# Optimization experiments

Hardware: AMD Instinct MI355X
Metric: run time of the kernel (lower is better)

The kernel has to match this reference:

```python
import jax, jax.numpy as jnp
import numpy as np

B, C, H, W = 16, 512, 32, 32
HW = H * W  # == input_features == output_features for shapes to be consistent


def setup_inputs() -> dict:
    key = jax.random.key(0)
    k1, k2, k3 = jax.random.split(key, 3)
    node1 = jax.random.normal(k1, (B, C, H, W), dtype=jnp.float32)
    node2 = jax.random.normal(k2, (B, C, H, W), dtype=jnp.float32)
    # nn.Linear(input_features, output_features, bias=False).weight: [out, in]
    W_c = jax.random.normal(k3, (HW, HW), dtype=jnp.float32) * (1.0 / np.sqrt(HW))
    return {"node1": node1, "node2": node2, "W_c": W_c}


def reference(node1, node2, W_c):
    b, c, h, w = node1.shape
    hw = h * w
    n1 = node1.reshape(b, c, hw)  # [B, C, HW]
    n2 = node2.reshape(b, c, hw)  # [B, C, HW]
    # x = W_c(n1): Linear applies y = x @ W^T  -> [B, C, HW_out]
    x = jnp.einsum('bch,oh->bco', n1, W_c)
    # e = bmm(x.permute(0,2,1), n2): [B, HW_out, C] @ [B, C, HW] -> [B, HW_out, HW]
    e = jnp.einsum('bco,bch->boh', x, n2)
    a = jax.nn.softmax(e, axis=-1)  # softmax over last dim (HW of node2)
    # m = bmm(n2, a): [B, C, HW] @ [B, HW, HW] -> [B, C, HW]
    m = jnp.einsum('bck,bkj->bcj', n2, a)
    return m
```

## Files before the change

kernel.cpp:

```cpp
#include <hip/hip_runtime.h>
#include <math.h>


typedef _Float16 f16;
typedef _Float16 f16x8 __attribute__((ext_vector_type(8)));
typedef _Float16 f16x4 __attribute__((ext_vector_type(4)));
typedef float f32x4 __attribute__((ext_vector_type(4)));

#define L2E 1.442695040888963f

#define WG_BARRIER() asm volatile("s_waitcnt lgkmcnt(0)\ns_barrier" ::: "memory")

#define DMA16(g, l)                                                             \
    __builtin_amdgcn_global_load_lds(                                           \
        (const __attribute__((address_space(1))) void*)(g),                     \
        (__attribute__((address_space(3))) void*)(l), 16, 0, 0)

__device__ __forceinline__ f16x8 cvt8(f32x4 lo, f32x4 hi) {
    f16x8 o;
#pragma unroll
    for (int i = 0; i < 4; ++i) { o[i] = (f16)lo[i]; o[4 + i] = (f16)hi[i]; }
    return o;
}

__device__ __forceinline__ f16x8 expb(f16x8 b, f32x4 cl, f32x4 ch) {
    f16x8 t;
#pragma unroll
    for (int i = 0; i < 4; ++i) t[i] = (f16)exp2f(fmaf((float)b[i], L2E, -cl[i]));
#pragma unroll
    for (int i = 0; i < 4; ++i) t[4 + i] = (f16)exp2f(fmaf((float)b[4 + i], L2E, -ch[i]));
    return t;
}

__global__ __launch_bounds__(256) void prep(const float* __restrict__ n1,
                                            const float* __restrict__ Wc,
                                            const float* __restrict__ n2,
                                            f16* __restrict__ n1f, f16* __restrict__ Wf,
                                            f16* __restrict__ n2t) {
    const int bid = blockIdx.x, tid = threadIdx.x;
    if (bid < 4608) {
        const float* s = (bid < 4096) ? n1 : Wc;
        f16* d = (bid < 4096) ? n1f : Wf;
        const size_t i = ((size_t)(bid < 4096 ? bid : bid - 4096) * 256 + tid) * 8;
        f32x4 a = *(const f32x4*)(s + i);
        f32x4 b = *(const f32x4*)(s + i + 4);
        *(f16x8*)(d + i) = cvt8(a, b);
        return;
    }
    const int id = bid - 4608;
    const int b = id >> 7;
    const int ry = (id & 127) >> 4;
    const int cx = id & 15;
    const float* S = n2 + (size_t)b * 512 * 1024;
    f16* Dt = n2t + (size_t)b * 1024 * 512;
    __shared__ f16 Ts[64 * 72];
    const int r0 = ry * 64, c0 = cx * 64;
    const int rr = tid >> 3, cc8 = (tid & 7) * 8;
#pragma unroll
    for (int h = 0; h < 2; ++h) {
        const int row = r0 + rr + 32 * h;
        const float* s = S + (size_t)row * 1024 + c0 + cc8;
        f32x4 a = *(const f32x4*)s, bq = *(const f32x4*)(s + 4);
        *(f16x8*)&Ts[(rr + 32 * h) * 72 + cc8] = cvt8(a, bq);
    }
    __syncthreads();
    const int j = tid >> 2, k16 = (tid & 3) * 16;
    f16* d = Dt + (size_t)(c0 + j) * 512 + r0 + k16;
    f16x8 o0, o1;
#pragma unroll
    for (int i = 0; i < 8; ++i) {
        o0[i] = Ts[(k16 + i) * 72 + j];
        o1[i] = Ts[(k16 + 8 + i) * 72 + j];
    }
    *(f16x8*)d = o0;
    *(f16x8*)(d + 8) = o1;
}

__global__ __launch_bounds__(256) void stats_combine(const float* __restrict__ Pm,
                                                     const float* __restrict__ Ps,
                                                     float* __restrict__ Sc) {
    const int g = blockIdx.x * 256 + threadIdx.x;
    const int b = g >> 10, o = g & 1023;
    const int mt = o >> 8, ml = o & 255;
    const float* pm = Pm + ((size_t)(b * 4 + mt) * 8) * 256 + ml;
    const float* ps = Ps + ((size_t)(b * 4 + mt) * 8) * 256 + ml;
    float M = -3.0e38f;
#pragma unroll
    for (int p = 0; p < 8; ++p) M = fmaxf(M, pm[p * 256]);
    float S = 0.f;
#pragma unroll
    for (int p = 0; p < 8; ++p) S += ps[p * 256] * exp2f(pm[p * 256] - M);
    Sc[g] = M + __log2f(S);
}

template <int NS>
__device__ __forceinline__ void gemm_dmac(const char* sA0, const char* sA1,
                                          const char* sB, char* dA, char* dB,
                                          char* SM, int wm, int wn, int col,
                                          int swz16, f32x4 (&acc)[4][4]) {
#pragma unroll
    for (int s = 0; s < 3; ++s) {
        if (s < NS) {
            const int o = s * 64;
            char* da = dA + s * 16384;
            char* db = dB + s * 8192;
            DMA16(sA0 + o, da); DMA16(sA1 + o, da + 8192); DMA16(sB + o, db);
        }
    }
#pragma unroll
    for (int kb = 0; kb < NS; ++kb) {
        if (kb + 2 < NS)      asm volatile("s_waitcnt vmcnt(6)" ::: "memory");
        else if (kb + 1 < NS) asm volatile("s_waitcnt vmcnt(3)" ::: "memory");
        else                  asm volatile("s_waitcnt vmcnt(0)" ::: "memory");
        __builtin_amdgcn_s_barrier();
        asm volatile("" ::: "memory");
        const char* Ac = SM + (kb % 3) * 16384;
        const char* Bc = SM + 49152 + (kb % 3) * 8192;
        f16x8 fa[4], fb[4];
#pragma unroll
        for (int u = 0; u < 4; ++u)
            fa[u] = *(const f16x8*)(Ac + (wm + u * 16 + col) * 64 + swz16);
#pragma unroll
        for (int v = 0; v < 4; ++v)
            fb[v] = *(const f16x8*)(Bc + (wn + v * 16 + col) * 64 + swz16);
        asm volatile("s_waitcnt lgkmcnt(0)" ::: "memory");
        __builtin_amdgcn_s_barrier();
        asm volatile("" ::: "memory");
        if (kb + 3 < NS) {
            const int o = (kb + 3) * 64;
            char* da = dA + (kb % 3) * 16384;
            char* db = dB + (kb % 3) * 8192;
            DMA16(sA0 + o, da); DMA16(sA1 + o, da + 8192); DMA16(sB + o, db);
        }
#pragma unroll
        for (int u = 0; u < 4; ++u)
#pragma unroll
            for (int v = 0; v < 4; ++v)
                acc[u][v] = __builtin_amdgcn_mfma_f32_16x16x32_f16(fa[u], fb[v],
                                                                   acc[u][v], 0, 0, 0);
    }
}

template <int NS, bool EXPB>
__device__ __forceinline__ void gemm_core_a32(const char* gA0, const char* gA1,
                                              const char* gB, const float* gSp,
                                              char* SM, int sOff, int wm, int wn,
                                              int col, int swz16, f32x4 (&acc)[4][4]) {
    f32x4 c00, c01, c10, c11;
    f32x4 a00l = *(const f32x4*)gA0, a00h = *(const f32x4*)(gA0 + 16);
    f32x4 a01l = *(const f32x4*)gA1, a01h = *(const f32x4*)(gA1 + 16);
    f16x8 b0 = *(const f16x8*)gB;
    if (EXPB) { c00 = *(const f32x4*)gSp; c01 = *(const f32x4*)(gSp + 4); }
    {
        char* dA = SM + sOff;
        *(f16x8*)dA = cvt8(a00l, a00h);
        *(f16x8*)(dA + 8192) = cvt8(a01l, a01h);
        char* dB = SM + 32768 + sOff;
        *(f16x8*)dB = EXPB ? expb(b0, c00, c01) : b0;
    }
    f32x4 a10l = *(const f32x4*)(gA0 + 128), a10h = *(const f32x4*)(gA0 + 144);
    f32x4 a11l = *(const f32x4*)(gA1 + 128), a11h = *(const f32x4*)(gA1 + 144);
    f16x8 b1 = *(const f16x8*)(gB + 64);
    if (EXPB) { c10 = *(const f32x4*)(gSp + 32); c11 = *(const f32x4*)(gSp + 36); }
    a00l = *(const f32x4*)(gA0 + 256); a00h = *(const f32x4*)(gA0 + 272);
    a01l = *(const f32x4*)(gA1 + 256); a01h = *(const f32x4*)(gA1 + 272);
    b0 = *(const f16x8*)(gB + 128);
    if (EXPB) { c00 = *(const f32x4*)(gSp + 64); c01 = *(const f32x4*)(gSp + 68); }
    WG_BARRIER();
#pragma unroll
    for (int kb = 0; kb < NS; ++kb) {
        const char* Ac = SM + (kb & 1) * 16384;
        const char* Bc = SM + 32768 + (kb & 1) * 8192;
        f16x8 fa[4], fb[4];
#pragma unroll
        for (int u = 0; u < 4; ++u)
            fa[u] = *(const f16x8*)(Ac + (wm + u * 16 + col) * 64 + swz16);
#pragma unroll
        for (int v = 0; v < 4; ++v)
            fb[v] = *(const f16x8*)(Bc + (wn + v * 16 + col) * 64 + swz16);
#pragma unroll
        for (int u = 0; u < 4; ++u)
#pragma unroll
            for (int v = 0; v < 4; ++v)
                acc[u][v] = __builtin_amdgcn_mfma_f32_16x16x32_f16(fa[u], fb[v],
                                                                   acc[u][v], 0, 0, 0);
        if (kb + 1 < NS) {
            char* dA = SM + ((kb + 1) & 1) * 16384 + sOff;
            char* dB = SM + 32768 + ((kb + 1) & 1) * 8192 + sOff;
            if ((kb & 1) == 0) {
                *(f16x8*)dA = cvt8(a10l, a10h);
                *(f16x8*)(dA + 8192) = cvt8(a11l, a11h);
                *(f16x8*)dB = EXPB ? expb(b1, c10, c11) : b1;
                if (kb + 3 < NS) {
                    a10l = *(const f32x4*)(gA0 + (size_t)(kb + 3) * 128);
                    a10h = *(const f32x4*)(gA0 + (size_t)(kb + 3) * 128 + 16);
                    a11l = *(const f32x4*)(gA1 + (size_t)(kb + 3) * 128);
                    a11h = *(const f32x4*)(gA1 + (size_t)(kb + 3) * 128 + 16);
                    b1 = *(const f16x8*)(gB + (size_t)(kb + 3) * 64);
                    if (EXPB) {
                        c10 = *(const f32x4*)(gSp + (size_t)(kb + 3) * 32);
                        c11 = *(const f32x4*)(gSp + (size_t)(kb + 3) * 32 + 4);
                    }
                }
            } else {
                *(f16x8*)dA = cvt8(a00l, a00h);
                *(f16x8*)(dA + 8192) = cvt8(a01l, a01h);
                *(f16x8*)dB = EXPB ? expb(b0, c00, c01) : b0;
                if (kb + 3 < NS) {
                    a00l = *(const f32x4*)(gA0 + (size_t)(kb + 3) * 128);
                    a00h = *(const f32x4*)(gA0 + (size_t)(kb + 3) * 128 + 16);
                    a01l = *(const f32x4*)(gA1 + (size_t)(kb + 3) * 128);
                    a01h = *(const f32x4*)(gA1 + (size_t)(kb + 3) * 128 + 16);
                    b0 = *(const f16x8*)(gB + (size_t)(kb + 3) * 64);
                    if (EXPB) {
                        c00 = *(const f32x4*)(gSp + (size_t)(kb + 3) * 32);
                        c01 = *(const f32x4*)(gSp + (size_t)(kb + 3) * 32 + 4);
                    }
                }
            }
            WG_BARRIER();
        }
    }
}

__device__ __forceinline__ void epilogue_tr(f32x4 (&acc)[4][4], char* SM, f16* dst0,
                                            int dstRow, int m0, int n0, int tid) {
    const int lane = tid & 63, wave = tid >> 6;
    const int col = lane & 15, quad = lane >> 4;
    const int wn = (wave >> 2) * 64;
    const int mh_w = (wave >> 1) & 1;
    const int wm_loc = (wave & 1) * 64;
    const int j = tid >> 2, seg = (tid & 3) * 32;
    WG_BARRIER();
    f16* Tt = (f16*)SM;
#pragma unroll
    for (int mh = 0; mh < 2; ++mh) {
        if (mh_w == mh) {
#pragma unroll
            for (int u = 0; u < 4; ++u)
#pragma unroll
                for (int v = 0; v < 4; ++v) {
                    f16x4 p;
#pragma unroll
                    for (int r = 0; r < 4; ++r) p[r] = (f16)acc[u][v][r];
                    *(f16x4*)&Tt[(wn + v * 16 + col) * 136 + wm_loc + u * 16 + quad * 4] = p;
                }
        }
        WG_BARRIER();
        f16* dst = dst0 + (size_t)(n0 + j) * dstRow + m0 + mh * 128 + seg;
#pragma unroll
        for (int c8 = 0; c8 < 32; c8 += 8)
            *(f16x8*)(dst + c8) = *(const f16x8*)&Tt[j * 136 + seg + c8];
        if (mh == 0) WG_BARRIER();
    }
}

__global__ __launch_bounds__(512) void gemm1_nt_xt(const f16* __restrict__ A,
                                                   const f16* __restrict__ Bw,
                                                   f16* __restrict__ Xt) {
    const int id = blockIdx.x;
    const int xcd = id & 7, loc = id >> 3;
    const int b = xcd * 2 + (loc >> 4);
    const int m0 = ((loc >> 3) & 1) * 256;
    const int n0 = (loc & 7) * 128;
    A += (size_t)b * 512 * 1024;
    Xt += (size_t)b * 1024 * 512;
    __shared__ __attribute__((aligned(16))) char SM[73728];
    const int tid = threadIdx.x, lane = tid & 63, wave = tid >> 6;
    const int col = lane & 15, quad = lane >> 4;
    const int wm = (wave & 3) * 64, wn = (wave >> 2) * 64;
    const int swz16 = (quad ^ ((col >> 1) & 3)) * 16;
    const int r = wave * 16 + (lane >> 2), ls = lane & 3;
    const int x = (r >> 1) & 3;
    const char* sA0 = (const char*)A + (size_t)(m0 + r) * 2048 + ((ls ^ x) * 16);
    const char* sA1 = sA0 + (size_t)128 * 2048;
    const char* sB  = (const char*)Bw + (size_t)(n0 + r) * 2048 + ((ls ^ x) * 16);
    char* dA = SM + wave * 1024;
    char* dB = SM + 49152 + wave * 1024;
    f32x4 acc[4][4] = {};
    gemm_dmac<32>(sA0, sA1, sB, dA, dB, SM, wm, wn, col, swz16, acc);
    epilogue_tr(acc, SM, Xt, 512, m0, n0, tid);
}

__global__ __launch_bounds__(512) void gemm2_nt_et(const f16* __restrict__ A,
                                                   const f16* __restrict__ B,
                                                   f16* __restrict__ Et,
                                                   float* __restrict__ Pm,
                                                   float* __restrict__ Ps) {
    const int id = blockIdx.x;
    const int xcd = id & 7, loc = id >> 3;
    const int b = xcd * 2 + (loc >> 5);
    const int m0 = ((loc >> 3) & 3) * 256;
    const int n0 = (loc & 7) * 128;
    A += (size_t)b * 1024 * 512;
    B += (size_t)b * 1024 * 512;
    Et += (size_t)b * 1024 * 1024;
    __shared__ __attribute__((aligned(16))) char SM[73728];
    const int tid = threadIdx.x, lane = tid & 63, wave = tid >> 6;
    const int col = lane & 15, quad = lane >> 4;
    const int wm = (wave & 3) * 64, wn = (wave >> 2) * 64;
    const int swz16 = (quad ^ ((col >> 1) & 3)) * 16;
    const int r = wave * 16 + (lane >> 2), ls = lane & 3;
    const int x = (r >> 1) & 3;
    const char* sA0 = (const char*)A + (size_t)(m0 + r) * 1024 + ((ls ^ x) * 16);
    const char* sA1 = sA0 + (size_t)128 * 1024;
    const char* sB  = (const char*)B + (size_t)(n0 + r) * 1024 + ((ls ^ x) * 16);
    char* dA = SM + wave * 1024;
    char* dB = SM + 49152 + wave * 1024;
    f32x4 acc[4][4] = {};
    gemm_dmac<16>(sA0, sA1, sB, dA, dB, SM, wm, wn, col, swz16, acc);

    {
        const int wn_e = (wave >> 2) * 64;
        const int mh_w = (wave >> 1) & 1;
        const int wm_loc = (wave & 1) * 64;
        const int j = tid >> 2, seg = (tid & 3) * 32;
        const int scol = tid >> 2, srq = tid & 3;
        WG_BARRIER();
        f16* Tt = (f16*)SM;
#pragma unroll
        for (int mh = 0; mh < 2; ++mh) {
            if (mh_w == mh) {
#pragma unroll
                for (int u = 0; u < 4; ++u)
#pragma unroll
                    for (int v = 0; v < 4; ++v) {
                        f16x4 p;
#pragma unroll
                        for (int r2 = 0; r2 < 4; ++r2) p[r2] = (f16)acc[u][v][r2];
                        *(f16x4*)&Tt[(wn_e + v * 16 + col) * 136 + wm_loc + u * 16 + quad * 4] = p;
                    }
            }
            WG_BARRIER();
            f16* dst = Et + (size_t)(n0 + j) * 1024 + m0 + mh * 128 + seg;
#pragma unroll
            for (int c8 = 0; c8 < 32; c8 += 8)
                *(f16x8*)(dst + c8) = *(const f16x8*)&Tt[j * 136 + seg + c8];
            float mx = -3.0e38f;
#pragma unroll
            for (int n = 0; n < 32; ++n) {
                const int row = srq * 32 + ((n + scol) & 31);
                mx = fmaxf(mx, (float)Tt[row * 136 + scol]);
            }
            const float mxl = mx * L2E;
            float s = 0.f;
#pragma unroll
            for (int n = 0; n < 32; ++n) {
                const int row = srq * 32 + ((n + scol) & 31);
                s += exp2f(fmaf((float)Tt[row * 136 + scol], L2E, -mxl));
            }
            float pmv = mxl, psv = s;
#pragma unroll
            for (int d = 1; d < 4; d <<= 1) {
                float om = __shfl_xor(pmv, d, 64);
                float os = __shfl_xor(psv, d, 64);
                float nm = fmaxf(pmv, om);
                psv = psv * exp2f(pmv - nm) + os * exp2f(om - nm);
                pmv = nm;
            }
            if (srq == 0) {
                const int part = (b * 4 + (m0 >> 8)) * 8 + (n0 >> 7);
                const int ml = mh * 128 + scol;
                Pm[(size_t)part * 256 + ml] = pmv;
                Ps[(size_t)part * 256 + ml] = psv;
            }
            if (mh == 0) WG_BARRIER();
        }
    }
}

__global__ __launch_bounds__(512) void gemm3_nt_out(const float* __restrict__ A,
                                                    const f16* __restrict__ Et,
                                                    const float* __restrict__ Sc,
                                                    float* __restrict__ C) {
    const int K = 1024;
    const int id = blockIdx.x;
    const int xcd = id & 7, loc = id >> 3;
    const int b = xcd * 2 + (loc >> 4);
    const int m0 = ((loc >> 3) & 1) * 256;
    const int n0 = (loc & 7) * 128;
    A += (size_t)b * 512 * K;
    Et += (size_t)b * 1024 * K;
    Sc += (size_t)b * 1024;
    C += (size_t)b * 512 * 1024;
    __shared__ __attribute__((aligned(16))) char SM[49152];
    const int tid = threadIdx.x, lane = tid & 63, wave = tid >> 6;
    const int col = lane & 15, quad = lane >> 4;
    const int wm = (wave & 3) * 64, wn = (wave >> 2) * 64;
    const int srow = tid >> 2, sslot = tid & 3;
    const int sOff = srow * 64 + ((sslot ^ ((srow >> 1) & 3)) * 16);
    const int swz16 = (quad ^ ((col >> 1) & 3)) * 16;
    const char* gA0 = (const char*)A + (size_t)(m0 + srow) * K * 4 + sslot * 32;
    const char* gA1 = gA0 + (size_t)128 * K * 4;
    const char* gB = (const char*)Et + (size_t)(n0 + srow) * K * 2 + sslot * 16;
    const float* gSp = Sc + sslot * 8;
    f32x4 acc[4][4] = {};
    gemm_core_a32<32, true>(gA0, gA1, gB, gSp, SM, sOff, wm, wn, col, swz16, acc);

#pragma unroll
    for (int u = 0; u < 4; ++u)
#pragma unroll
        for (int v = 0; v < 4; ++v)
#pragma unroll
            for (int r = 0; r < 4; ++r)
                C[(size_t)(m0 + wm + u * 16 + quad * 4 + r) * 1024 + n0 + wn + v * 16 + col] =
                    acc[u][v][r];
}

extern "C" void kernel_launch(void* const* d_in, const int* in_sizes, int n_in,
                              void* d_out, int out_size, void* d_ws, size_t ws_size,
                              hipStream_t stream) {
    const float* n1 = (const float*)d_in[0];
    const float* n2 = (const float*)d_in[1];
    const float* Wc = (const float*)d_in[2];
    float* out = (float*)d_out;
    char* ws = (char*)d_ws;

    f16* n2t = (f16*)(ws);
    f16* Xt  = (f16*)(ws + (16u << 20));
    f16* Wf  = (f16*)(ws + (32u << 20));
    f16* Et  = (f16*)(ws + (32u << 20));
    f16* n1f = (f16*)(ws + (64u << 20));
    float* Pm = (float*)(ws + (80u << 20));
    float* Ps = (float*)(ws + (81u << 20));
    float* Sc = (float*)(ws + (82u << 20));

    prep<<<6656, dim3(256), 0, stream>>>(n1, Wc, n2, n1f, Wf, n2t);
    gemm1_nt_xt<<<256, dim3(512), 0, stream>>>(n1f, Wf, Xt);
    gemm2_nt_et<<<512, dim3(512), 0, stream>>>(Xt, n2t, Et, Pm, Ps);
    stats_combine<<<64, dim3(256), 0, stream>>>(Pm, Ps, Sc);
    gemm3_nt_out<<<256, dim3(512), 0, stream>>>(n2, Et, Sc, out);
}
```

Measured before the change: 197.5 us.

## Feed gemm3 from fp16 n2 copy via async LDS DMA with in-LDS exp

New measurement: 195.4 us. Within noise of the previous version (-1.1%).

```diff
diff --git a/kernel.cpp b/kernel.cpp
--- a/kernel.cpp
+++ b/kernel.cpp
@@ -36,7 +36,7 @@
                                             const float* __restrict__ Wc,
                                             const float* __restrict__ n2,
                                             f16* __restrict__ n1f, f16* __restrict__ Wf,
-                                            f16* __restrict__ n2t) {
+                                            f16* __restrict__ n2f, f16* __restrict__ n2t) {
     const int bid = blockIdx.x, tid = threadIdx.x;
     if (bid < 4608) {
         const float* s = (bid < 4096) ? n1 : Wc;
@@ -52,6 +52,7 @@
     const int ry = (id & 127) >> 4;
     const int cx = id & 15;
     const float* S = n2 + (size_t)b * 512 * 1024;
+    f16* Dn = n2f + (size_t)b * 512 * 1024;
     f16* Dt = n2t + (size_t)b * 1024 * 512;
     __shared__ f16 Ts[64 * 72];
     const int r0 = ry * 64, c0 = cx * 64;
@@ -61,7 +62,9 @@
         const int row = r0 + rr + 32 * h;
         const float* s = S + (size_t)row * 1024 + c0 + cc8;
         f32x4 a = *(const f32x4*)s, bq = *(const f32x4*)(s + 4);
-        *(f16x8*)&Ts[(rr + 32 * h) * 72 + cc8] = cvt8(a, bq);
+        f16x8 o = cvt8(a, bq);
+        *(f16x8*)&Ts[(rr + 32 * h) * 72 + cc8] = o;
+        *(f16x8*)(Dn + (size_t)row * 1024 + c0 + cc8) = o;
     }
     __syncthreads();
     const int j = tid >> 2, k16 = (tid & 3) * 16;
@@ -141,85 +144,61 @@
     }
 }
 
-template <int NS, bool EXPB>
-__device__ __forceinline__ void gemm_core_a32(const char* gA0, const char* gA1,
-                                              const char* gB, const float* gSp,
-                                              char* SM, int sOff, int wm, int wn,
-                                              int col, int swz16, f32x4 (&acc)[4][4]) {
-    f32x4 c00, c01, c10, c11;
-    f32x4 a00l = *(const f32x4*)gA0, a00h = *(const f32x4*)(gA0 + 16);
-    f32x4 a01l = *(const f32x4*)gA1, a01h = *(const f32x4*)(gA1 + 16);
-    f16x8 b0 = *(const f16x8*)gB;
-    if (EXPB) { c00 = *(const f32x4*)gSp; c01 = *(const f32x4*)(gSp + 4); }
-    {
-        char* dA = SM + sOff;
-        *(f16x8*)dA = cvt8(a00l, a00h);
-        *(f16x8*)(dA + 8192) = cvt8(a01l, a01h);
-        char* dB = SM + 32768 + sOff;
-        *(f16x8*)dB = EXPB ? expb(b0, c00, c01) : b0;
-    }
-    f32x4 a10l = *(const f32x4*)(gA0 + 128), a10h = *(const f32x4*)(gA0 + 144);
-    f32x4 a11l = *(const f32x4*)(gA1 + 128), a11h = *(const f32x4*)(gA1 + 144);
-    f16x8 b1 = *(const f16x8*)(gB + 64);
-    if (EXPB) { c10 = *(const f32x4*)(gSp + 32); c11 = *(const f32x4*)(gSp + 36); }
-    a00l = *(const f32x4*)(gA0 + 256); a00h = *(const f32x4*)(gA0 + 272);
-    a01l = *(const f32x4*)(gA1 + 256); a01h = *(const f32x4*)(gA1 + 272);
-    b0 = *(const f16x8*)(gB + 128);
-    if (EXPB) { c00 = *(const f32x4*)(gSp + 64); c01 = *(const f32x4*)(gSp + 68); }
-    WG_BARRIER();
+template <int NS>
+__device__ __forceinline__ void gemm_dmac_exp(const char* sA0, const char* sA1,
+                                              const char* sB, char* dA, char* dB,
+                                              char* SM, int wm, int wn, int col,
+                                              int swz16, int slotOff, int kloc,
+                                              f32x4 (&acc)[4][4]) {
+    const float* scL = (const float*)(SM + 90112);
+#pragma unroll
+    for (int s = 0; s < 3; ++s) {
+        if (s < NS) {
+            const int o = s * 64;
+            char* da = dA + s * 16384;
+            char* db = dB + s * 8192;
+            DMA16(sA0 + o, da); DMA16(sA1 + o, da + 8192); DMA16(sB + o, db);
+        }
+    }
 #pragma unroll
     for (int kb = 0; kb < NS; ++kb) {
-        const char* Ac = SM + (kb & 1) * 16384;
-        const char* Bc = SM + 32768 + (kb & 1) * 8192;
-        f16x8 fa[4], fb[4];
+        if (kb + 2 < NS)      asm volatile("s_waitcnt vmcnt(6)" ::: "memory");
+        else if (kb + 1 < NS) asm volatile("s_waitcnt vmcnt(3)" ::: "memory");
+        else                  asm volatile("s_waitcnt vmcnt(0)" ::: "memory");
+        __builtin_amdgcn_s_barrier();
+        asm volatile("" ::: "memory");
+        const char* Ac = SM + (kb % 3) * 16384;
+        const char* Braw = SM + 49152 + (kb % 3) * 8192;
+        char* Bexp = SM + 73728 + (kb & 1) * 8192;
+        f16x8 fa[4];
 #pragma unroll
         for (int u = 0; u < 4; ++u)
             fa[u] = *(const f16x8*)(Ac + (wm + u * 16 + col) * 64 + swz16);
+        {
+            f16x8 raw = *(const f16x8*)(Braw + slotOff);
+            f32x4 s0 = *(const f32x4*)(scL + kb * 32 + kloc);
+            f32x4 s1 = *(const f32x4*)(scL + kb * 32 + kloc + 4);
+            *(f16x8*)(Bexp + slotOff) = expb(raw, s0, s1);
+        }
+        asm volatile("s_waitcnt lgkmcnt(0)" ::: "memory");
+        __builtin_amdgcn_s_barrier();
+        asm volatile("" ::: "memory");
+        if (kb + 3 < NS) {
+            const int o = (kb + 3) * 64;
+            char* da = dA + (kb % 3) * 16384;
+            char* db = dB + (kb % 3) * 8192;
+            DMA16(sA0 + o, da); DMA16(sA1 + o, da + 8192); DMA16(sB + o, db);
+        }
+        f16x8 fb[4];
 #pragma unroll
         for (int v = 0; v < 4; ++v)
-            fb[v] = *(const f16x8*)(Bc + (wn + v * 16 + col) * 64 + swz16);
+            fb[v] = *(const f16x8*)(Bexp + (wn + v * 16 + col) * 64 + swz16);
 #pragma unroll
         for (int u = 0; u < 4; ++u)
 #pragma unroll
             for (int v = 0; v < 4; ++v)
                 acc[u][v] = __builtin_amdgcn_mfma_f32_16x16x32_f16(fa[u], fb[v],
                                                                    acc[u][v], 0, 0, 0);
-        if (kb + 1 < NS) {
-            char* dA = SM + ((kb + 1) & 1) * 16384 + sOff;
-            char* dB = SM + 32768 + ((kb + 1) & 1) * 8192 + sOff;
-            if ((kb & 1) == 0) {
-                *(f16x8*)dA = cvt8(a10l, a10h);
-                *(f16x8*)(dA + 8192) = cvt8(a11l, a11h);
-                *(f16x8*)dB = EXPB ? expb(b1, c10, c11) : b1;
-                if (kb + 3 < NS) {
-                    a10l = *(const f32x4*)(gA0 + (size_t)(kb + 3) * 128);
-                    a10h = *(const f32x4*)(gA0 + (size_t)(kb + 3) * 128 + 16);
-                    a11l = *(const f32x4*)(gA1 + (size_t)(kb + 3) * 128);
-                    a11h = *(const f32x4*)(gA1 + (size_t)(kb + 3) * 128 + 16);
-                    b1 = *(const f16x8*)(gB + (size_t)(kb + 3) * 64);
-                    if (EXPB) {
-                        c10 = *(const f32x4*)(gSp + (size_t)(kb + 3) * 32);
-                        c11 = *(const f32x4*)(gSp + (size_t)(kb + 3) * 32 + 4);
-                    }
-                }
-            } else {
-                *(f16x8*)dA = cvt8(a00l, a00h);
-                *(f16x8*)(dA + 8192) = cvt8(a01l, a01h);
-                *(f16x8*)dB = EXPB ? expb(b0, c00, c01) : b0;
-                if (kb + 3 < NS) {
-                    a00l = *(const f32x4*)(gA0 + (size_t)(kb + 3) * 128);
-                    a00h = *(const f32x4*)(gA0 + (size_t)(kb + 3) * 128 + 16);
-                    a01l = *(const f32x4*)(gA1 + (size_t)(kb + 3) * 128);
-                    a01h = *(const f32x4*)(gA1 + (size_t)(kb + 3) * 128 + 16);
-                    b0 = *(const f16x8*)(gB + (size_t)(kb + 3) * 64);
-                    if (EXPB) {
-                        c00 = *(const f32x4*)(gSp + (size_t)(kb + 3) * 32);
-                        c01 = *(const f32x4*)(gSp + (size_t)(kb + 3) * 32 + 4);
-                    }
-                }
-            }
-            WG_BARRIER();
-        }
     }
 }
 
@@ -369,42 +348,55 @@
     }
 }
 
-__global__ __launch_bounds__(512) void gemm3_nt_out(const float* __restrict__ A,
+__global__ __launch_bounds__(512) void gemm3_nt_out(const f16* __restrict__ A,
                                                     const f16* __restrict__ Et,
                                                     const float* __restrict__ Sc,
                                                     float* __restrict__ C) {
-    const int K = 1024;
     const int id = blockIdx.x;
     const int xcd = id & 7, loc = id >> 3;
     const int b = xcd * 2 + (loc >> 4);
     const int m0 = ((loc >> 3) & 1) * 256;
     const int n0 = (loc & 7) * 128;
-    A += (size_t)b * 512 * K;
-    Et += (size_t)b * 1024 * K;
+    A += (size_t)b * 512 * 1024;
+    Et += (size_t)b * 1024 * 1024;
     Sc += (size_t)b * 1024;
     C += (size_t)b * 512 * 1024;
-    __shared__ __attribute__((aligned(16))) char SM[49152];
+    __shared__ __attribute__((aligned(16))) char SM[94208];
     const int tid = threadIdx.x, lane = tid & 63, wave = tid >> 6;
     const int col = lane & 15, quad = lane >> 4;
     const int wm = (wave & 3) * 64, wn = (wave >> 2) * 64;
-    const int srow = tid >> 2, sslot = tid & 3;
-    const int sOff = srow * 64 + ((sslot ^ ((srow >> 1) & 3)) * 16);
     const int swz16 = (quad ^ ((col >> 1) & 3)) * 16;
-    const char* gA0 = (const char*)A + (size_t)(m0 + srow) * K * 4 + sslot * 32;
-    const char* gA1 = gA0 + (size_t)128 * K * 4;
-    const char* gB = (const char*)Et + (size_t)(n0 + srow) * K * 2 + sslot * 16;
-    const float* gSp = Sc + sslot * 8;
+    const int r = wave * 16 + (lane >> 2), ls = lane & 3;
+    const int x = (r >> 1) & 3;
+    const char* sA0 = (const char*)A + (size_t)(m0 + r) * 2048 + ((ls ^ x) * 16);
+    const char* sA1 = sA0 + (size_t)128 * 2048;
+    const char* sB  = (const char*)Et + (size_t)(n0 + r) * 2048 + ((ls ^ x) * 16);
+    char* dA = SM + wave * 1024;
+    char* dB = SM + 49152 + wave * 1024;
+    const int slotOff = r * 64 + ls * 16;
+    const int kloc = (ls ^ x) * 8;
+
+    {
+        float* scL = (float*)(SM + 90112);
+        if (tid < 256) {
+            f32x4 v = *(const f32x4*)(Sc + tid * 4);
+            *(f32x4*)(scL + tid * 4) = v;
+        }
+        WG_BARRIER();
+    }
+
     f32x4 acc[4][4] = {};
-    gemm_core_a32<32, true>(gA0, gA1, gB, gSp, SM, sOff, wm, wn, col, swz16, acc);
+    gemm_dmac_exp<32>(sA0, sA1, sB, dA, dB, SM, wm, wn, col, swz16,
+                      slotOff, kloc, acc);
 
 #pragma unroll
     for (int u = 0; u < 4; ++u)
 #pragma unroll
         for (int v = 0; v < 4; ++v)
 #pragma unroll
-            for (int r = 0; r < 4; ++r)
-                C[(size_t)(m0 + wm + u * 16 + quad * 4 + r) * 1024 + n0 + wn + v * 16 + col] =
-                    acc[u][v][r];
+            for (int r2 = 0; r2 < 4; ++r2)
+                C[(size_t)(m0 + wm + u * 16 + quad * 4 + r2) * 1024 + n0 + wn + v * 16 + col] =
+                    acc[u][v][r2];
 }
 
 extern "C" void kernel_launch(void* const* d_in, const int* in_sizes, int n_in,
@@ -421,13 +413,14 @@
     f16* Wf  = (f16*)(ws + (32u << 20));
     f16* Et  = (f16*)(ws + (32u << 20));
     f16* n1f = (f16*)(ws + (64u << 20));
-    float* Pm = (float*)(ws + (80u << 20));
-    float* Ps = (float*)(ws + (81u << 20));
-    float* Sc = (float*)(ws + (82u << 20));
-
-    prep<<<6656, dim3(256), 0, stream>>>(n1, Wc, n2, n1f, Wf, n2t);
+    f16* n2f = (f16*)(ws + (80u << 20));
+    float* Pm = (float*)(ws + (64u << 20));
+    float* Ps = (float*)(ws + (65u << 20));
+    float* Sc = (float*)(ws + (66u << 20));
+
+    prep<<<6656, dim3(256), 0, stream>>>(n1, Wc, n2, n1f, Wf, n2f, n2t);
     gemm1_nt_xt<<<256, dim3(512), 0, stream>>>(n1f, Wf, Xt);
     gemm2_nt_et<<<512, dim3(512), 0, stream>>>(Xt, n2t, Et, Pm, Ps);
     stats_combine<<<64, dim3(256), 0, stream>>>(Pm, Ps, Sc);
-    gemm3_nt_out<<<256, dim3(512), 0, stream>>>(n2, Et, Sc, out);
-}
+    gemm3_nt_out<<<256, dim3(512), 0, stream>>>(n2f, Et, Sc, out);
+}
```
